# Optimization experiments

Hardware: AMD Instinct MI355X
Metric: run time of the kernel (lower is better)

Reference implementation:

```python
import jax, jax.numpy as jnp
import numpy as np

V_IN, E, H, V_OUT = 32000, 512, 1024, 50257


def setup_inputs() -> dict:
    key = jax.random.key(0)
    ks = jax.random.split(key, 12)
    g = lambda k, shape: (jax.random.normal(k, shape, dtype=jnp.float32) * 0.05)
    return {
        "state": jax.random.randint(ks[0], (1, 2048), 0, V_IN),
        "max_len": 512,
        "emb": g(ks[1], (V_IN, E)),
        "enc_Wih": g(ks[2], (4 * H, E)),
        "enc_Whh": g(ks[3], (4 * H, H)),
        "enc_bih": g(ks[4], (4 * H,)),
        "enc_bhh": g(ks[5], (4 * H,)),
        "dec_Wih": g(ks[6], (4 * H, 1)),
        "dec_Whh": g(ks[7], (4 * H, H)),
        "dec_bih": g(ks[8], (4 * H,)),
        "dec_bhh": g(ks[9], (4 * H,)),
        "Wout": g(ks[10], (V_OUT, H)),
        "bout": g(ks[11], (V_OUT,)),
    }


def _lstm_cell(h, c, gates):
    # PyTorch gate order: i, f, g, o
    i, f, g, o = jnp.split(gates, 4)
    i = jax.nn.sigmoid(i)
    f = jax.nn.sigmoid(f)
    g = jnp.tanh(g)
    o = jax.nn.sigmoid(o)
    c = f * c + i * g
    h = o * jnp.tanh(c)
    return h, c


def reference(state, max_len, emb, enc_Wih, enc_Whh, enc_bih, enc_bhh,
              dec_Wih, dec_Whh, dec_bih, dec_bhh, Wout, bout):
    hdim = enc_Whh.shape[1]
    # ---- encoder: embed tokens, run LSTM over seq (batch = 1) ----
    xs = emb[state[0]]  # [S, E]
    enc_b = enc_bih + enc_bhh

    def enc_step(carry, x):
        h, c = carry
        gates = enc_Wih @ x + enc_Whh @ h + enc_b  # [4H]
        return _lstm_cell(h, c, gates), None

    z = jnp.zeros((hdim,), dtype=emb.dtype)
    (h, c), _ = jax.lax.scan(enc_step, (z, z), xs)

    # ---- decoder: input is always zeros(1,1,1), so Wih contributes 0 ----
    dec_b = dec_bih + dec_bhh + dec_Wih[:, 0] * 0.0

    def dec_step(carry, _):
        h, c = carry
        gates = dec_Whh @ h + dec_b
        h, c = _lstm_cell(h, c, gates)
        probs = jax.nn.softmax(Wout @ h + bout)  # [V_out]
        return (h, c), probs

    _, probs = jax.lax.scan(dec_step, (h, c), None, length=max_len)
    return probs[None]  # [1, max_len, V_out]
```

## Files before the change

### kernel.cpp

```cpp
#include <hip/hip_runtime.h>
#include <stdint.h>
#include <math.h>


typedef __attribute__((ext_vector_type(8))) short short8;
typedef __attribute__((ext_vector_type(4))) float f32x4;
typedef unsigned long long u64;

#define HD 1024
#define ED 512
#define TPB 256
#define RNN_TPB 512
#define RNN_NWG 128
#define UPW 8
#define SENT32 0x7F7F7F7Fu

#define AGT __HIP_MEMORY_SCOPE_AGENT
#define RLX __ATOMIC_RELAXED

__device__ __forceinline__ unsigned short f2bf(float f) {
  union { float f; unsigned u; } x; x.f = f;
  unsigned u = x.u;
  u += 0x7fffu + ((u >> 16) & 1u);
  return (unsigned short)(u >> 16);
}
__device__ __forceinline__ float frcp(float x) { return __builtin_amdgcn_rcpf(x); }
__device__ __forceinline__ float fsig(float x) { return frcp(1.0f + __expf(-x)); }
__device__ __forceinline__ float ftanh(float x) { return 1.0f - 2.0f * frcp(1.0f + __expf(2.0f * x)); }

__global__ __launch_bounds__(RNN_TPB)
void rnn_kernel(const int* __restrict__ state,
                const float* __restrict__ emb,
                const float* __restrict__ encWih,
                const float* __restrict__ encWhh,
                const float* __restrict__ encbih,
                const float* __restrict__ encbhh,
                const float* __restrict__ decWhh,
                const float* __restrict__ decbih,
                const float* __restrict__ decbhh,
                unsigned int* __restrict__ hbuf,
                unsigned short* __restrict__ Adec,
                int S, int T) {
  __shared__ __align__(16) float vec[HD + ED];

  const int tid = threadIdx.x;
  const int wg  = blockIdx.x;
  const int w   = tid >> 6;
  const int c   = tid & 63;
  const int u   = wg * UPW + w;

  float4 wh[4][4];
  float4 wx[4][2];
  float4 br;
#pragma unroll
  for (int g = 0; g < 4; ++g) {
    const size_t rb = (size_t)(g * HD + u);
#pragma unroll
    for (int j = 0; j < 4; ++j)
      wh[g][j] = *(const float4*)&encWhh[rb * HD + 4 * (c + 64 * j)];
#pragma unroll
    for (int j = 0; j < 2; ++j)
      wx[g][j] = *(const float4*)&encWih[rb * ED + 4 * (c + 64 * j)];
  }
  br.x = encbih[0 * HD + u] + encbhh[0 * HD + u];
  br.y = encbih[1 * HD + u] + encbhh[1 * HD + u];
  br.z = encbih[2 * HD + u] + encbhh[2 * HD + u];
  br.w = encbih[3 * HD + u] + encbhh[3 * HD + u];

  float4 xreg;
  if (tid >= 256 && tid < 384) {
    int tok = state[0];
    xreg = *(const float4*)&emb[(size_t)tok * ED + 4 * (tid - 256)];
  }

  float cs = 0.0f;

  for (int t = 0; t < S + T; ++t) {
    const bool dec = (t >= S);
    if (t == S) {
#pragma unroll
      for (int g = 0; g < 4; ++g) {
        const size_t rb = (size_t)(g * HD + u);
#pragma unroll
        for (int j = 0; j < 4; ++j)
          wh[g][j] = *(const float4*)&decWhh[rb * HD + 4 * (c + 64 * j)];
      }
      br.x = decbih[0 * HD + u] + decbhh[0 * HD + u];
      br.y = decbih[1 * HD + u] + decbhh[1 * HD + u];
      br.z = decbih[2 * HD + u] + decbhh[2 * HD + u];
      br.w = decbih[3 * HD + u] + decbhh[3 * HD + u];
    }

    if (tid < 256) {
      if (t == 0) {
        *(float4*)&vec[4 * tid] = make_float4(0.f, 0.f, 0.f, 0.f);
      } else {
        const u64* L = (const u64*)hbuf + (((size_t)(t & 3)) << 9) + tid * 2;
        u64 d0, d1;
        do {
          d0 = __hip_atomic_load(&L[0], RLX, AGT);
          d1 = __hip_atomic_load(&L[1], RLX, AGT);
        } while ((unsigned)d0 == SENT32 || (unsigned)(d0 >> 32) == SENT32 ||
                 (unsigned)d1 == SENT32 || (unsigned)(d1 >> 32) == SENT32);
        union { u64 u[2]; float4 f; } p;
        p.u[0] = d0; p.u[1] = d1;
        *(float4*)&vec[4 * tid] = p.f;
      }
    } else if (tid < 384) {
      if (!dec) {
        *(float4*)&vec[HD + 4 * (tid - 256)] = xreg;
        if (t + 1 < S) {
          int tok = state[t + 1];
          xreg = *(const float4*)&emb[(size_t)tok * ED + 4 * (tid - 256)];
        }
      }
    }
    __syncthreads();

    if (c == 0)
      __hip_atomic_store(&hbuf[(size_t)((t + 2) & 3) * HD + u], SENT32, RLX, AGT);

    float a0 = 0.f, a1 = 0.f, a2 = 0.f, a3 = 0.f;
#pragma unroll
    for (int j = 0; j < 4; ++j) {
      float4 v = *(const float4*)&vec[4 * (c + 64 * j)];
      a0 = fmaf(wh[0][j].x, v.x, fmaf(wh[0][j].y, v.y, fmaf(wh[0][j].z, v.z, fmaf(wh[0][j].w, v.w, a0))));
      a1 = fmaf(wh[1][j].x, v.x, fmaf(wh[1][j].y, v.y, fmaf(wh[1][j].z, v.z, fmaf(wh[1][j].w, v.w, a1))));
      a2 = fmaf(wh[2][j].x, v.x, fmaf(wh[2][j].y, v.y, fmaf(wh[2][j].z, v.z, fmaf(wh[2][j].w, v.w, a2))));
      a3 = fmaf(wh[3][j].x, v.x, fmaf(wh[3][j].y, v.y, fmaf(wh[3][j].z, v.z, fmaf(wh[3][j].w, v.w, a3))));
    }
    if (!dec) {
#pragma unroll
      for (int j = 0; j < 2; ++j) {
        float4 v = *(const float4*)&vec[HD + 4 * (c + 64 * j)];
        a0 = fmaf(wx[0][j].x, v.x, fmaf(wx[0][j].y, v.y, fmaf(wx[0][j].z, v.z, fmaf(wx[0][j].w, v.w, a0))));
        a1 = fmaf(wx[1][j].x, v.x, fmaf(wx[1][j].y, v.y, fmaf(wx[1][j].z, v.z, fmaf(wx[1][j].w, v.w, a1))));
        a2 = fmaf(wx[2][j].x, v.x, fmaf(wx[2][j].y, v.y, fmaf(wx[2][j].z, v.z, fmaf(wx[2][j].w, v.w, a2))));
        a3 = fmaf(wx[3][j].x, v.x, fmaf(wx[3][j].y, v.y, fmaf(wx[3][j].z, v.z, fmaf(wx[3][j].w, v.w, a3))));
      }
    }
#pragma unroll
    for (int off = 1; off < 64; off <<= 1) {
      a0 += __shfl_xor(a0, off);
      a1 += __shfl_xor(a1, off);
      a2 += __shfl_xor(a2, off);
      a3 += __shfl_xor(a3, off);
    }

    float iv = fsig(a0 + br.x);
    float fv = fsig(a1 + br.y);
    float gv = ftanh(a2 + br.z);
    float ov = fsig(a3 + br.w);
    cs = fv * cs + iv * gv;
    float hv = ov * ftanh(cs);

    if (c == 0) {
      asm volatile("s_waitcnt vmcnt(0)" ::: "memory");
      union { float f; unsigned u; } x; x.f = hv;
      __hip_atomic_store(&hbuf[(size_t)((t + 1) & 3) * HD + u], x.u, RLX, AGT);
      if (dec) Adec[(size_t)(t - S) * HD + u] = f2bf(hv);
    }
    __syncthreads();
  }
}

#define AST 56

__global__ __launch_bounds__(TPB)
void out_gemm(const unsigned short* __restrict__ Adec,
              const float* __restrict__ Wout,
              const float* __restrict__ bout,
              float* __restrict__ out,
              int V) {
  __shared__ __align__(16) unsigned short Alds[512 * AST];
  const int tid  = threadIdx.x;
  const int wv   = tid >> 6;
  const int lane = tid & 63;
  const int col  = lane & 15;
  const int quad = lane >> 4;
  const int v0   = blockIdx.x * 64;

  f32x4 acc[4][8];
#pragma unroll
  for (int bt = 0; bt < 4; ++bt)
#pragma unroll
    for (int tt = 0; tt < 8; ++tt)
      acc[bt][tt] = (f32x4){0.f, 0.f, 0.f, 0.f};

  for (int k0 = 0; k0 < HD; k0 += 32) {
    __syncthreads();
#pragma unroll
    for (int i = 0; i < 8; ++i) {
      int id = tid + (i << 8);
      int rt = id >> 2, c4 = id & 3;
      uint4 d = *(const uint4*)(Adec + rt * HD + k0 + (c4 << 3));
      *(uint4*)&Alds[rt * AST + (c4 << 3)] = d;
    }
    __syncthreads();
    short8 bf[4];
#pragma unroll
    for (int bt = 0; bt < 4; ++bt) {
      int v = v0 + (bt << 4) + col;
      if (v >= V) v = V - 1;
      const float4* wp = (const float4*)(Wout + (size_t)v * HD + k0 + (quad << 3));
      float4 w0 = wp[0], w1 = wp[1];
      short8 b;
      b[0] = (short)f2bf(w0.x); b[1] = (short)f2bf(w0.y);
      b[2] = (short)f2bf(w0.z); b[3] = (short)f2bf(w0.w);
      b[4] = (short)f2bf(w1.x); b[5] = (short)f2bf(w1.y);
      b[6] = (short)f2bf(w1.z); b[7] = (short)f2bf(w1.w);
      bf[bt] = b;
    }
#pragma unroll
    for (int tt = 0; tt < 8; ++tt) {
      int trow = (wv << 7) + (tt << 4) + col;
      short8 af = *(const short8*)&Alds[trow * AST + (quad << 3)];
#pragma unroll
      for (int bt = 0; bt < 4; ++bt)
        acc[bt][tt] = __builtin_amdgcn_mfma_f32_16x16x32_bf16(af, bf[bt], acc[bt][tt], 0, 0, 0);
    }
  }
#pragma unroll
  for (int bt = 0; bt < 4; ++bt) {
    int v = v0 + (bt << 4) + col;
    if (v < V) {
      float bb = bout[v];
#pragma unroll
      for (int tt = 0; tt < 8; ++tt) {
        int tb = (wv << 7) + (tt << 4) + (quad << 2);
        f32x4 a = acc[bt][tt];
        out[(size_t)(tb + 0) * V + v] = a[0] + bb;
        out[(size_t)(tb + 1) * V + v] = a[1] + bb;
        out[(size_t)(tb + 2) * V + v] = a[2] + bb;
        out[(size_t)(tb + 3) * V + v] = a[3] + bb;
      }
    }
  }
}

__global__ __launch_bounds__(TPB)
void softmax_rows(float* __restrict__ out, int V) {
  float* rowp = out + (size_t)blockIdx.x * V;
  __shared__ float red[8];
  const int tid = threadIdx.x;

  float m = -1e30f;
  for (int v = tid; v < V; v += TPB) m = fmaxf(m, rowp[v]);
#pragma unroll
  for (int off = 32; off >= 1; off >>= 1) m = fmaxf(m, __shfl_xor(m, off));
  if ((tid & 63) == 0) red[tid >> 6] = m;
  __syncthreads();
  if (tid == 0) red[4] = fmaxf(fmaxf(red[0], red[1]), fmaxf(red[2], red[3]));
  __syncthreads();
  m = red[4];

  float s = 0.0f;
  for (int v = tid; v < V; v += TPB) {
    float e = expf(rowp[v] - m);
    rowp[v] = e;
    s += e;
  }
#pragma unroll
  for (int off = 32; off >= 1; off >>= 1) s += __shfl_xor(s, off);
  if ((tid & 63) == 0) red[tid >> 6] = s;
  __syncthreads();
  if (tid == 0) red[5] = red[0] + red[1] + red[2] + red[3];
  __syncthreads();
  float inv = 1.0f / red[5];
  for (int v = tid; v < V; v += TPB) rowp[v] *= inv;
}

extern "C" void kernel_launch(void* const* d_in, const int* in_sizes, int n_in,
                              void* d_out, int out_size, void* d_ws, size_t ws_size,
                              hipStream_t stream) {
  const int*   state  = (const int*)d_in[0];
  const float* emb    = (const float*)d_in[2];
  const float* encWih = (const float*)d_in[3];
  const float* encWhh = (const float*)d_in[4];
  const float* encbih = (const float*)d_in[5];
  const float* encbhh = (const float*)d_in[6];
  const float* decWhh = (const float*)d_in[8];
  const float* decbih = (const float*)d_in[9];
  const float* decbhh = (const float*)d_in[10];
  const float* Wout   = (const float*)d_in[11];
  const float* bout   = (const float*)d_in[12];
  float*       out    = (float*)d_out;

  const int S = in_sizes[0];
  const int V = in_sizes[12];
  const int T = out_size / V;

  hipMemsetAsync(d_ws, 0x7F, 16384, stream);
  unsigned int*   hbuf = (unsigned int*)d_ws;
  unsigned short* Adec = (unsigned short*)((char*)d_ws + 65536);

  rnn_kernel<<<RNN_NWG, RNN_TPB, 0, stream>>>(state, emb, encWih, encWhh, encbih, encbhh,
                                              decWhh, decbih, decbhh, hbuf, Adec, S, T);
  int nvb = (V + 63) / 64;
  out_gemm<<<nvb, TPB, 0, stream>>>(Adec, Wout, bout, out, V);
  softmax_rows<<<T, TPB, 0, stream>>>(out, V);
}
```

Measured before the change: 8.441 ms.

## Halve RNN workgroups by assigning two hidden units per wave

The persistent LSTM kernel now runs on 64 workgroups instead of 128, and each wave computes two hidden units, so it holds 48 float4 weight registers instead of 24. This reduces the number of agents polling and publishing in the cross-workgroup hbuf exchange each step. The h writes are gathered through shared memory and issued by 16 lanes per workgroup. The embedding prefetch into registers is removed and the row is loaded directly each step. The trade-offs are higher register pressure with possible spills, twice the FMA work per wave, and an embedding load that now sits on the critical path.

```diff
diff --git a/kernel.cpp b/kernel.cpp
--- a/kernel.cpp
+++ b/kernel.cpp
@@ -11,8 +11,7 @@
 #define ED 512
 #define TPB 256
 #define RNN_TPB 512
-#define RNN_NWG 128
-#define UPW 8
+#define RNN_NWG 64
 #define SENT32 0x7F7F7F7Fu
 
 #define AGT __HIP_MEMORY_SCOPE_AGENT
@@ -27,6 +26,9 @@
 __device__ __forceinline__ float frcp(float x) { return __builtin_amdgcn_rcpf(x); }
 __device__ __forceinline__ float fsig(float x) { return frcp(1.0f + __expf(-x)); }
 __device__ __forceinline__ float ftanh(float x) { return 1.0f - 2.0f * frcp(1.0f + __expf(2.0f * x)); }
+
+#define DOT4(a, W, v) \
+  a = fmaf((W).x, (v).x, fmaf((W).y, (v).y, fmaf((W).z, (v).z, fmaf((W).w, (v).w, (a)))))
 
 __global__ __launch_bounds__(RNN_TPB)
 void rnn_kernel(const int* __restrict__ state,
@@ -42,60 +44,66 @@
                 unsigned short* __restrict__ Adec,
                 int S, int T) {
   __shared__ __align__(16) float vec[HD + ED];
+  __shared__ float gsh[16];
 
   const int tid = threadIdx.x;
   const int wg  = blockIdx.x;
-  const int w   = tid >> 6;
+  const int wv  = tid >> 6;
   const int c   = tid & 63;
-  const int u   = wg * UPW + w;
-
-  float4 wh[4][4];
-  float4 wx[4][2];
-  float4 br;
+  const int uA  = (wg << 4) + wv;
+  const int uB  = uA + 8;
+
+  float4 w[48];
 #pragma unroll
   for (int g = 0; g < 4; ++g) {
-    const size_t rb = (size_t)(g * HD + u);
-#pragma unroll
-    for (int j = 0; j < 4; ++j)
-      wh[g][j] = *(const float4*)&encWhh[rb * HD + 4 * (c + 64 * j)];
-#pragma unroll
-    for (int j = 0; j < 2; ++j)
-      wx[g][j] = *(const float4*)&encWih[rb * ED + 4 * (c + 64 * j)];
-  }
-  br.x = encbih[0 * HD + u] + encbhh[0 * HD + u];
-  br.y = encbih[1 * HD + u] + encbhh[1 * HD + u];
-  br.z = encbih[2 * HD + u] + encbhh[2 * HD + u];
-  br.w = encbih[3 * HD + u] + encbhh[3 * HD + u];
-
-  float4 xreg;
-  if (tid >= 256 && tid < 384) {
-    int tok = state[0];
-    xreg = *(const float4*)&emb[(size_t)tok * ED + 4 * (tid - 256)];
-  }
-
-  float cs = 0.0f;
+#pragma unroll
+    for (int j = 0; j < 4; ++j) {
+      w[g * 4 + j]      = *(const float4*)&encWhh[((size_t)(g * HD) + uA) * HD + 4 * (c + 64 * j)];
+      w[16 + g * 4 + j] = *(const float4*)&encWhh[((size_t)(g * HD) + uB) * HD + 4 * (c + 64 * j)];
+    }
+#pragma unroll
+    for (int j = 0; j < 2; ++j) {
+      w[32 + g * 2 + j] = *(const float4*)&encWih[((size_t)(g * HD) + uA) * ED + 4 * (c + 64 * j)];
+      w[40 + g * 2 + j] = *(const float4*)&encWih[((size_t)(g * HD) + uB) * ED + 4 * (c + 64 * j)];
+    }
+  }
+  float4 brA, brB;
+  brA.x = encbih[0 * HD + uA] + encbhh[0 * HD + uA];
+  brA.y = encbih[1 * HD + uA] + encbhh[1 * HD + uA];
+  brA.z = encbih[2 * HD + uA] + encbhh[2 * HD + uA];
+  brA.w = encbih[3 * HD + uA] + encbhh[3 * HD + uA];
+  brB.x = encbih[0 * HD + uB] + encbhh[0 * HD + uB];
+  brB.y = encbih[1 * HD + uB] + encbhh[1 * HD + uB];
+  brB.z = encbih[2 * HD + uB] + encbhh[2 * HD + uB];
+  brB.w = encbih[3 * HD + uB] + encbhh[3 * HD + uB];
+
+  float csA = 0.0f, csB = 0.0f;
 
   for (int t = 0; t < S + T; ++t) {
     const bool dec = (t >= S);
     if (t == S) {
 #pragma unroll
-      for (int g = 0; g < 4; ++g) {
-        const size_t rb = (size_t)(g * HD + u);
-#pragma unroll
-        for (int j = 0; j < 4; ++j)
-          wh[g][j] = *(const float4*)&decWhh[rb * HD + 4 * (c + 64 * j)];
-      }
-      br.x = decbih[0 * HD + u] + decbhh[0 * HD + u];
-      br.y = decbih[1 * HD + u] + decbhh[1 * HD + u];
-      br.z = decbih[2 * HD + u] + decbhh[2 * HD + u];
-      br.w = decbih[3 * HD + u] + decbhh[3 * HD + u];
+      for (int g = 0; g < 4; ++g)
+#pragma unroll
+        for (int j = 0; j < 4; ++j) {
+          w[g * 4 + j]      = *(const float4*)&decWhh[((size_t)(g * HD) + uA) * HD + 4 * (c + 64 * j)];
+          w[16 + g * 4 + j] = *(const float4*)&decWhh[((size_t)(g * HD) + uB) * HD + 4 * (c + 64 * j)];
+        }
+      brA.x = decbih[0 * HD + uA] + decbhh[0 * HD + uA];
+      brA.y = decbih[1 * HD + uA] + decbhh[1 * HD + uA];
+      brA.z = decbih[2 * HD + uA] + decbhh[2 * HD + uA];
+      brA.w = decbih[3 * HD + uA] + decbhh[3 * HD + uA];
+      brB.x = decbih[0 * HD + uB] + decbhh[0 * HD + uB];
+      brB.y = decbih[1 * HD + uB] + decbhh[1 * HD + uB];
+      brB.z = decbih[2 * HD + uB] + decbhh[2 * HD + uB];
+      brB.w = decbih[3 * HD + uB] + decbhh[3 * HD + uB];
     }
 
     if (tid < 256) {
       if (t == 0) {
         *(float4*)&vec[4 * tid] = make_float4(0.f, 0.f, 0.f, 0.f);
       } else {
-        const u64* L = (const u64*)hbuf + (((size_t)(t & 3)) << 9) + tid * 2;
+        const u64* L = (const u64*)hbuf + (((size_t)(t & 3)) << 9) + (tid << 1);
         u64 d0, d1;
         do {
           d0 = __hip_atomic_load(&L[0], RLX, AGT);
@@ -108,59 +116,62 @@
       }
     } else if (tid < 384) {
       if (!dec) {
-        *(float4*)&vec[HD + 4 * (tid - 256)] = xreg;
-        if (t + 1 < S) {
-          int tok = state[t + 1];
-          xreg = *(const float4*)&emb[(size_t)tok * ED + 4 * (tid - 256)];
-        }
+        int tok = state[t];
+        *(float4*)&vec[HD + 4 * (tid - 256)] =
+            *(const float4*)&emb[(size_t)tok * ED + 4 * (tid - 256)];
       }
     }
     __syncthreads();
 
-    if (c == 0)
-      __hip_atomic_store(&hbuf[(size_t)((t + 2) & 3) * HD + u], SENT32, RLX, AGT);
-
-    float a0 = 0.f, a1 = 0.f, a2 = 0.f, a3 = 0.f;
+    if (tid < 16)
+      __hip_atomic_store(&hbuf[(size_t)((t + 2) & 3) * HD + (wg << 4) + tid], SENT32, RLX, AGT);
+
+    float acc[8] = {0.f, 0.f, 0.f, 0.f, 0.f, 0.f, 0.f, 0.f};
 #pragma unroll
     for (int j = 0; j < 4; ++j) {
       float4 v = *(const float4*)&vec[4 * (c + 64 * j)];
-      a0 = fmaf(wh[0][j].x, v.x, fmaf(wh[0][j].y, v.y, fmaf(wh[0][j].z, v.z, fmaf(wh[0][j].w, v.w, a0))));
-      a1 = fmaf(wh[1][j].x, v.x, fmaf(wh[1][j].y, v.y, fmaf(wh[1][j].z, v.z, fmaf(wh[1][j].w, v.w, a1))));
-      a2 = fmaf(wh[2][j].x, v.x, fmaf(wh[2][j].y, v.y, fmaf(wh[2][j].z, v.z, fmaf(wh[2][j].w, v.w, a2))));
-      a3 = fmaf(wh[3][j].x, v.x, fmaf(wh[3][j].y, v.y, fmaf(wh[3][j].z, v.z, fmaf(wh[3][j].w, v.w, a3))));
+#pragma unroll
+      for (int g = 0; g < 4; ++g) {
+        DOT4(acc[g],     w[g * 4 + j],      v);
+        DOT4(acc[4 + g], w[16 + g * 4 + j], v);
+      }
     }
     if (!dec) {
 #pragma unroll
       for (int j = 0; j < 2; ++j) {
         float4 v = *(const float4*)&vec[HD + 4 * (c + 64 * j)];
-        a0 = fmaf(wx[0][j].x, v.x, fmaf(wx[0][j].y, v.y, fmaf(wx[0][j].z, v.z, fmaf(wx[0][j].w, v.w, a0))));
-        a1 = fmaf(wx[1][j].x, v.x, fmaf(wx[1][j].y, v.y, fmaf(wx[1][j].z, v.z, fmaf(wx[1][j].w, v.w, a1))));
-        a2 = fmaf(wx[2][j].x, v.x, fmaf(wx[2][j].y, v.y, fmaf(wx[2][j].z, v.z, fmaf(wx[2][j].w, v.w, a2))));
-        a3 = fmaf(wx[3][j].x, v.x, fmaf(wx[3][j].y, v.y, fmaf(wx[3][j].z, v.z, fmaf(wx[3][j].w, v.w, a3))));
-      }
-    }
-#pragma unroll
-    for (int off = 1; off < 64; off <<= 1) {
-      a0 += __shfl_xor(a0, off);
-      a1 += __shfl_xor(a1, off);
-      a2 += __shfl_xor(a2, off);
-      a3 += __shfl_xor(a3, off);
-    }
-
-    float iv = fsig(a0 + br.x);
-    float fv = fsig(a1 + br.y);
-    float gv = ftanh(a2 + br.z);
-    float ov = fsig(a3 + br.w);
-    cs = fv * cs + iv * gv;
-    float hv = ov * ftanh(cs);
-
-    if (c == 0) {
+#pragma unroll
+        for (int g = 0; g < 4; ++g) {
+          DOT4(acc[g],     w[32 + g * 2 + j], v);
+          DOT4(acc[4 + g], w[40 + g * 2 + j], v);
+        }
+      }
+    }
+#pragma unroll
+    for (int off = 1; off < 64; off <<= 1)
+#pragma unroll
+      for (int q = 0; q < 8; ++q)
+        acc[q] += __shfl_xor(acc[q], off);
+
+    float iA = fsig(acc[0] + brA.x), fA = fsig(acc[1] + brA.y);
+    float gA = ftanh(acc[2] + brA.z), oA = fsig(acc[3] + brA.w);
+    csA = fA * csA + iA * gA;
+    float hA = oA * ftanh(csA);
+    float iB = fsig(acc[4] + brB.x), fB = fsig(acc[5] + brB.y);
+    float gB = ftanh(acc[6] + brB.z), oB = fsig(acc[7] + brB.w);
+    csB = fB * csB + iB * gB;
+    float hB = oB * ftanh(csB);
+
+    if (c == 0) { gsh[wv] = hA; gsh[wv + 8] = hB; }
+    __syncthreads();
+
+    if (tid < 16) {
+      float hv = gsh[tid];
       asm volatile("s_waitcnt vmcnt(0)" ::: "memory");
       union { float f; unsigned u; } x; x.f = hv;
-      __hip_atomic_store(&hbuf[(size_t)((t + 1) & 3) * HD + u], x.u, RLX, AGT);
-      if (dec) Adec[(size_t)(t - S) * HD + u] = f2bf(hv);
-    }
-    __syncthreads();
+      __hip_atomic_store(&hbuf[(size_t)((t + 1) & 3) * HD + (wg << 4) + tid], x.u, RLX, AGT);
+      if (dec) Adec[(size_t)(t - S) * HD + (wg << 4) + tid] = f2bf(hv);
+    }
   }
 }
 
```

After: 21.05 ms. +149.4%, slower.

## Halve RNN workgroups, two hidden units per wave with merged reduction

Applied to the files above, without the earlier changes.

The persistent LSTM kernel now runs on 64 workgroups instead of 128. Each wave keeps the weights for two hidden units in registers, 48 float4 per lane. The cross-lane reduction uses a butterfly merge that folds 8 gate sums into one value per lane group, and it goes through shared memory so 16 threads finish the cell update. The polling load is a single dwordx4 inline-asm load with sc0 sc1 in place of two 64-bit atomics. Fewer workgroups means fewer participants in the grid-wide handshake each step, at the cost of high register pressure and an extra __syncthreads per step.

```diff
diff --git a/kernel.cpp b/kernel.cpp
--- a/kernel.cpp
+++ b/kernel.cpp
@@ -5,14 +5,15 @@
 
 typedef __attribute__((ext_vector_type(8))) short short8;
 typedef __attribute__((ext_vector_type(4))) float f32x4;
+typedef __attribute__((ext_vector_type(4))) unsigned int u32x4;
 typedef unsigned long long u64;
+typedef unsigned int u32;
 
 #define HD 1024
 #define ED 512
 #define TPB 256
 #define RNN_TPB 512
-#define RNN_NWG 128
-#define UPW 8
+#define RNN_NWG 64
 #define SENT32 0x7F7F7F7Fu
 
 #define AGT __HIP_MEMORY_SCOPE_AGENT
@@ -28,7 +29,13 @@
 __device__ __forceinline__ float fsig(float x) { return frcp(1.0f + __expf(-x)); }
 __device__ __forceinline__ float ftanh(float x) { return 1.0f - 2.0f * frcp(1.0f + __expf(2.0f * x)); }
 
-__global__ __launch_bounds__(RNN_TPB)
+#define DOT4(a, W, v) \
+  a = fmaf((W).x, (v).x, fmaf((W).y, (v).y, fmaf((W).z, (v).z, fmaf((W).w, (v).w, (a)))))
+
+#define MRG2(r, a, b, m) { float _sa = __shfl_xor((a), (m)), _sb = __shfl_xor((b), (m)); \
+                           (r) = (lane & (m)) ? ((b) + _sb) : ((a) + _sa); }
+
+__global__ __launch_bounds__(RNN_TPB, 2)
 void rnn_kernel(const int* __restrict__ state,
                 const float* __restrict__ emb,
                 const float* __restrict__ encWih,
@@ -38,72 +45,80 @@
                 const float* __restrict__ decWhh,
                 const float* __restrict__ decbih,
                 const float* __restrict__ decbhh,
-                unsigned int* __restrict__ hbuf,
+                u32* __restrict__ hbuf,
                 unsigned short* __restrict__ Adec,
                 int S, int T) {
   __shared__ __align__(16) float vec[HD + ED];
-
-  const int tid = threadIdx.x;
-  const int wg  = blockIdx.x;
-  const int w   = tid >> 6;
-  const int c   = tid & 63;
-  const int u   = wg * UPW + w;
-
-  float4 wh[4][4];
-  float4 wx[4][2];
-  float4 br;
+  __shared__ __align__(16) float gshf[64];
+
+  const int tid  = threadIdx.x;
+  const int wg   = blockIdx.x;
+  const int w    = tid >> 6;
+  const int lane = tid & 63;
+  const int uA   = (wg << 4) + (w << 1);
+
+  float4 wr[48];
 #pragma unroll
   for (int g = 0; g < 4; ++g) {
-    const size_t rb = (size_t)(g * HD + u);
-#pragma unroll
-    for (int j = 0; j < 4; ++j)
-      wh[g][j] = *(const float4*)&encWhh[rb * HD + 4 * (c + 64 * j)];
-#pragma unroll
-    for (int j = 0; j < 2; ++j)
-      wx[g][j] = *(const float4*)&encWih[rb * ED + 4 * (c + 64 * j)];
-  }
-  br.x = encbih[0 * HD + u] + encbhh[0 * HD + u];
-  br.y = encbih[1 * HD + u] + encbhh[1 * HD + u];
-  br.z = encbih[2 * HD + u] + encbhh[2 * HD + u];
-  br.w = encbih[3 * HD + u] + encbhh[3 * HD + u];
-
-  float4 xreg;
+#pragma unroll
+    for (int j = 0; j < 4; ++j) {
+      wr[g * 4 + j]      = *(const float4*)&encWhh[((size_t)(g * HD) + uA) * HD + 4 * (lane + 64 * j)];
+      wr[16 + g * 4 + j] = *(const float4*)&encWhh[((size_t)(g * HD) + uA + 1) * HD + 4 * (lane + 64 * j)];
+    }
+#pragma unroll
+    for (int j = 0; j < 2; ++j) {
+      wr[32 + g * 2 + j] = *(const float4*)&encWih[((size_t)(g * HD) + uA) * ED + 4 * (lane + 64 * j)];
+      wr[40 + g * 2 + j] = *(const float4*)&encWih[((size_t)(g * HD) + uA + 1) * ED + 4 * (lane + 64 * j)];
+    }
+  }
+
+  float4 bias = {0.f, 0.f, 0.f, 0.f};
+  float cs = 0.0f;
+  if (tid < 16) {
+    int u = (wg << 4) + tid;
+    bias.x = encbih[u]          + encbhh[u];
+    bias.y = encbih[HD + u]     + encbhh[HD + u];
+    bias.z = encbih[2 * HD + u] + encbhh[2 * HD + u];
+    bias.w = encbih[3 * HD + u] + encbhh[3 * HD + u];
+  }
+
+  float4 xreg = {0.f, 0.f, 0.f, 0.f};
   if (tid >= 256 && tid < 384) {
     int tok = state[0];
     xreg = *(const float4*)&emb[(size_t)tok * ED + 4 * (tid - 256)];
   }
 
-  float cs = 0.0f;
-
   for (int t = 0; t < S + T; ++t) {
     const bool dec = (t >= S);
     if (t == S) {
 #pragma unroll
-      for (int g = 0; g < 4; ++g) {
-        const size_t rb = (size_t)(g * HD + u);
-#pragma unroll
-        for (int j = 0; j < 4; ++j)
-          wh[g][j] = *(const float4*)&decWhh[rb * HD + 4 * (c + 64 * j)];
-      }
-      br.x = decbih[0 * HD + u] + decbhh[0 * HD + u];
-      br.y = decbih[1 * HD + u] + decbhh[1 * HD + u];
-      br.z = decbih[2 * HD + u] + decbhh[2 * HD + u];
-      br.w = decbih[3 * HD + u] + decbhh[3 * HD + u];
+      for (int g = 0; g < 4; ++g)
+#pragma unroll
+        for (int j = 0; j < 4; ++j) {
+          wr[g * 4 + j]      = *(const float4*)&decWhh[((size_t)(g * HD) + uA) * HD + 4 * (lane + 64 * j)];
+          wr[16 + g * 4 + j] = *(const float4*)&decWhh[((size_t)(g * HD) + uA + 1) * HD + 4 * (lane + 64 * j)];
+        }
+      if (tid < 16) {
+        int u = (wg << 4) + tid;
+        bias.x = decbih[u]          + decbhh[u];
+        bias.y = decbih[HD + u]     + decbhh[HD + u];
+        bias.z = decbih[2 * HD + u] + decbhh[2 * HD + u];
+        bias.w = decbih[3 * HD + u] + decbhh[3 * HD + u];
+      }
     }
 
     if (tid < 256) {
       if (t == 0) {
         *(float4*)&vec[4 * tid] = make_float4(0.f, 0.f, 0.f, 0.f);
       } else {
-        const u64* L = (const u64*)hbuf + (((size_t)(t & 3)) << 9) + tid * 2;
-        u64 d0, d1;
+        const u32* L = hbuf + (((size_t)(t & 3)) << 10) + (tid << 2);
+        u32x4 d;
         do {
-          d0 = __hip_atomic_load(&L[0], RLX, AGT);
-          d1 = __hip_atomic_load(&L[1], RLX, AGT);
-        } while ((unsigned)d0 == SENT32 || (unsigned)(d0 >> 32) == SENT32 ||
-                 (unsigned)d1 == SENT32 || (unsigned)(d1 >> 32) == SENT32);
-        union { u64 u[2]; float4 f; } p;
-        p.u[0] = d0; p.u[1] = d1;
+          asm volatile("global_load_dwordx4 %0, %1, off sc0 sc1\n\t"
+                       "s_waitcnt vmcnt(0)"
+                       : "=v"(d) : "v"(L) : "memory");
+        } while (d.x == SENT32 || d.y == SENT32 || d.z == SENT32 || d.w == SENT32);
+        union { u32x4 u; float4 f; } p; p.u = d;
         *(float4*)&vec[4 * tid] = p.f;
       }
     } else if (tid < 384) {
@@ -117,50 +132,53 @@
     }
     __syncthreads();
 
-    if (c == 0)
-      __hip_atomic_store(&hbuf[(size_t)((t + 2) & 3) * HD + u], SENT32, RLX, AGT);
+    if (tid < 16)
+      __hip_atomic_store(&hbuf[(((size_t)((t + 2) & 3)) << 10) + (wg << 4) + tid], SENT32, RLX, AGT);
 
     float a0 = 0.f, a1 = 0.f, a2 = 0.f, a3 = 0.f;
+    float a4 = 0.f, a5 = 0.f, a6 = 0.f, a7 = 0.f;
 #pragma unroll
     for (int j = 0; j < 4; ++j) {
-      float4 v = *(const float4*)&vec[4 * (c + 64 * j)];
-      a0 = fmaf(wh[0][j].x, v.x, fmaf(wh[0][j].y, v.y, fmaf(wh[0][j].z, v.z, fmaf(wh[0][j].w, v.w, a0))));
-      a1 = fmaf(wh[1][j].x, v.x, fmaf(wh[1][j].y, v.y, fmaf(wh[1][j].z, v.z, fmaf(wh[1][j].w, v.w, a1))));
-      a2 = fmaf(wh[2][j].x, v.x, fmaf(wh[2][j].y, v.y, fmaf(wh[2][j].z, v.z, fmaf(wh[2][j].w, v.w, a2))));
-      a3 = fmaf(wh[3][j].x, v.x, fmaf(wh[3][j].y, v.y, fmaf(wh[3][j].z, v.z, fmaf(wh[3][j].w, v.w, a3))));
+      float4 v = *(const float4*)&vec[4 * (lane + 64 * j)];
+      DOT4(a0, wr[0 * 4 + j], v);  DOT4(a1, wr[1 * 4 + j], v);
+      DOT4(a2, wr[2 * 4 + j], v);  DOT4(a3, wr[3 * 4 + j], v);
+      DOT4(a4, wr[16 + 0 * 4 + j], v);  DOT4(a5, wr[16 + 1 * 4 + j], v);
+      DOT4(a6, wr[16 + 2 * 4 + j], v);  DOT4(a7, wr[16 + 3 * 4 + j], v);
     }
     if (!dec) {
 #pragma unroll
       for (int j = 0; j < 2; ++j) {
-        float4 v = *(const float4*)&vec[HD + 4 * (c + 64 * j)];
-        a0 = fmaf(wx[0][j].x, v.x, fmaf(wx[0][j].y, v.y, fmaf(wx[0][j].z, v.z, fmaf(wx[0][j].w, v.w, a0))));
-        a1 = fmaf(wx[1][j].x, v.x, fmaf(wx[1][j].y, v.y, fmaf(wx[1][j].z, v.z, fmaf(wx[1][j].w, v.w, a1))));
-        a2 = fmaf(wx[2][j].x, v.x, fmaf(wx[2][j].y, v.y, fmaf(wx[2][j].z, v.z, fmaf(wx[2][j].w, v.w, a2))));
-        a3 = fmaf(wx[3][j].x, v.x, fmaf(wx[3][j].y, v.y, fmaf(wx[3][j].z, v.z, fmaf(wx[3][j].w, v.w, a3))));
-      }
-    }
-#pragma unroll
-    for (int off = 1; off < 64; off <<= 1) {
-      a0 += __shfl_xor(a0, off);
-      a1 += __shfl_xor(a1, off);
-      a2 += __shfl_xor(a2, off);
-      a3 += __shfl_xor(a3, off);
-    }
-
-    float iv = fsig(a0 + br.x);
-    float fv = fsig(a1 + br.y);
-    float gv = ftanh(a2 + br.z);
-    float ov = fsig(a3 + br.w);
-    cs = fv * cs + iv * gv;
-    float hv = ov * ftanh(cs);
-
-    if (c == 0) {
+        float4 v = *(const float4*)&vec[HD + 4 * (lane + 64 * j)];
+        DOT4(a0, wr[32 + 0 * 2 + j], v);  DOT4(a1, wr[32 + 1 * 2 + j], v);
+        DOT4(a2, wr[32 + 2 * 2 + j], v);  DOT4(a3, wr[32 + 3 * 2 + j], v);
+        DOT4(a4, wr[40 + 0 * 2 + j], v);  DOT4(a5, wr[40 + 1 * 2 + j], v);
+        DOT4(a6, wr[40 + 2 * 2 + j], v);  DOT4(a7, wr[40 + 3 * 2 + j], v);
+      }
+    }
+    float m0, m1, m2, m3, n0, n1, vv;
+    MRG2(m0, a0, a1, 1);  MRG2(m1, a2, a3, 1);
+    MRG2(m2, a4, a5, 1);  MRG2(m3, a6, a7, 1);
+    MRG2(n0, m0, m1, 2);  MRG2(n1, m2, m3, 2);
+    MRG2(vv, n0, n1, 4);
+    vv += __shfl_xor(vv, 8);
+    vv += __shfl_xor(vv, 16);
+    vv += __shfl_xor(vv, 32);
+    if (lane < 8) gshf[8 * w + lane] = vv;
+    __syncthreads();
+
+    if (tid < 16) {
+      float4 gs = *(const float4*)&gshf[4 * tid];
+      float iv = fsig(gs.x + bias.x);
+      float fv = fsig(gs.y + bias.y);
+      float gv = ftanh(gs.z + bias.z);
+      float ov = fsig(gs.w + bias.w);
+      cs = fv * cs + iv * gv;
+      float hv = ov * ftanh(cs);
       asm volatile("s_waitcnt vmcnt(0)" ::: "memory");
-      union { float f; unsigned u; } x; x.f = hv;
-      __hip_atomic_store(&hbuf[(size_t)((t + 1) & 3) * HD + u], x.u, RLX, AGT);
-      if (dec) Adec[(size_t)(t - S) * HD + u] = f2bf(hv);
-    }
-    __syncthreads();
+      union { float f; u32 u; } x; x.f = hv;
+      __hip_atomic_store(&hbuf[(((size_t)((t + 1) & 3)) << 10) + (wg << 4) + tid], x.u, RLX, AGT);
+      if (dec) Adec[(size_t)(t - S) * HD + (wg << 4) + tid] = f2bf(hv);
+    }
   }
 }
 
@@ -291,7 +309,7 @@
   const int T = out_size / V;
 
   hipMemsetAsync(d_ws, 0x7F, 16384, stream);
-  unsigned int*   hbuf = (unsigned int*)d_ws;
+  u32*            hbuf = (u32*)d_ws;
   unsigned short* Adec = (unsigned short*)((char*)d_ws + 65536);
 
   rnn_kernel<<<RNN_NWG, RNN_TPB, 0, stream>>>(state, emb, encWih, encWhh, encbih, encbhh,
```

Result: slower. 11.19 ms (+32.5%).
